# Kernel optimization log

Hardware: AMD Instinct MI355X
Metric: run time of the kernel (lower is better)

Reference implementation:

```python
import jax, jax.numpy as jnp
import numpy as np

EMB = 512
HEADS = 8
HD = EMB // HEADS
DEPTH = 6
CONT = 100
CAT_DIMS = [100] * 28
CAT = len(CAT_DIMS)
HID = int(EMB * (4.0 / 3.0))  # 682, FT-Transformer ReGLU hidden
B = 128
OFFSETS = jnp.asarray(np.concatenate([[0], np.cumsum(CAT_DIMS[:-1])]).astype(np.int32))
SQRT_EMB = float(np.sqrt(EMB))  # scores are DIVIDED by emb**-0.5 in the source


def setup_inputs() -> dict:
    key = jax.random.key(0)
    ks = jax.random.split(key, 16)
    s = 0.02
    x_cat = jax.random.randint(ks[0], (B, CAT), 0, CAT_DIMS[0]).astype(jnp.float32)
    x_cont = jax.random.normal(ks[1], (B, CONT), dtype=jnp.float32)
    x = jnp.concatenate([x_cat, x_cont], axis=1)  # [B, CAT+CONT]
    return {
        "x": x,
        "tok_w": jax.random.normal(ks[2], (CONT + 1, EMB)) * s,
        "tok_b": jax.random.normal(ks[3], (CONT + CAT, EMB)) * s,
        "cat_emb": jax.random.normal(ks[4], (sum(CAT_DIMS), EMB)) * s,
        "Wqkv": jax.random.normal(ks[5], (DEPTH, EMB, 3 * EMB)) * s,
        "bqkv": jnp.zeros((DEPTH, 3 * EMB)),
        "Wout": jax.random.normal(ks[6], (DEPTH, EMB, EMB)) * s,
        "bout": jnp.zeros((DEPTH, EMB)),
        "W0": jax.random.normal(ks[7], (DEPTH, EMB, 2 * HID)) * s,
        "b0": jnp.zeros((DEPTH, 2 * HID)),
        "W1": jax.random.normal(ks[8], (DEPTH, HID, EMB)) * s,
        "b1": jnp.zeros((DEPTH, EMB)),
        "ln0_g": jnp.ones((DEPTH, EMB)),
        "ln0_b": jnp.zeros((DEPTH, EMB)),
        "ln1_g": jnp.ones((DEPTH, EMB)),
        "ln1_b": jnp.zeros((DEPTH, EMB)),
    }


def _ln(x, g, b):
    m = x.mean(-1, keepdims=True)
    v = x.var(-1, keepdims=True)
    return (x - m) / jnp.sqrt(v + 1e-5) * g + b


def _attn(x, Wqkv, bqkv, Wout, bout):
    Bn, S, _ = x.shape
    # faithful layout: reshape to (B,S,H,3*hd), move heads, chunk last dim
    qkv = (x @ Wqkv + bqkv).reshape(Bn, S, HEADS, 3 * HD).transpose(0, 2, 1, 3)
    q, k, v = jnp.split(qkv, 3, axis=-1)  # each [B,H,S,hd]
    scores = jnp.einsum("bhqd,bhkd->bhqk", q, k) * SQRT_EMB  # / (emb**-0.5)
    attn = jax.nn.softmax(jax.nn.softmax(scores, axis=-1), axis=-1)  # double softmax, as in source
    o = jnp.einsum("bhqk,bhkd->bhqd", attn, v)
    o = o.transpose(0, 2, 1, 3).reshape(Bn, S, EMB)
    return o @ Wout + bout


def _reglu(x):
    a, b = jnp.split(x, 2, axis=-1)
    return a * jax.nn.relu(b)


def _forward(x, tok_w, tok_b, cat_emb, Wqkv, bqkv, Wout, bout, W0, b0, W1, b1,
             ln0_g, ln0_b, ln1_g, ln1_b):
    # --- feature tokenizer ---
    x_cats = x[:, :CAT].astype(jnp.int32)
    x_conts = jnp.concatenate([jnp.ones((x.shape[0], 1), x.dtype), x[:, CAT:]], axis=1)  # [B, CONT+1]
    h = tok_w[None] * x_conts[:, :, None]  # [B, CONT+1, EMB]
    h = jnp.concatenate([h, cat_emb[x_cats + OFFSETS[None]]], axis=1)  # [B, S=129, EMB]
    bias = jnp.concatenate([jnp.zeros((1, EMB), h.dtype), tok_b], axis=0)
    h = h + bias[None]
    # --- transformer stack ---
    for i in range(DEPTH):
        xin = _ln(h, ln0_g[i], ln0_b[i]) if i else h  # layer 0 has no norm0
        h = h + _attn(xin, Wqkv[i], bqkv[i], Wout[i], bout[i])
        r = _ln(h, ln1_g[i], ln1_b[i])
        r = _reglu(r @ W0[i] + b0[i]) @ W1[i] + b1[i]
        h = h + r
    return h[:, 0]  # CLS token


def reference(x, tok_w, tok_b, cat_emb, Wqkv, bqkv, Wout, bout, W0, b0, W1, b1,
              ln0_g, ln0_b, ln1_g, ln1_b):
    return _forward(x, tok_w, tok_b, cat_emb, Wqkv, bqkv, Wout, bout, W0, b0, W1, b1,
                    ln0_g, ln0_b, ln1_g, ln1_b)
```

## Files before the change

### kernel.cpp

```cpp
#include <hip/hip_runtime.h>
#include <hip/hip_bf16.h>
#include <stdint.h>


typedef __hip_bfloat16 bf16_t;
typedef __attribute__((ext_vector_type(8))) __bf16 bf16x8;
typedef __attribute__((ext_vector_type(4))) float floatx4;

constexpr int M_ROWS = 16512;
constexpr float SQRT_EMB_F = 22.627416997969522f;

__device__ __forceinline__ floatx4 mfma16(bf16x8 a, bf16x8 b, floatx4 c) {
  return __builtin_amdgcn_mfma_f32_16x16x32_bf16(a, b, c, 0, 0, 0);
}

__device__ __forceinline__ size_t frag_chunk(int m, int k, int KT) {
  return ((size_t)(m >> 4) * KT + (k >> 5)) * 512 + (m & 15) * 8 + 128 * ((k >> 3) & 3);
}
__device__ __forceinline__ size_t frag_elem(int m, int k, int KT) {
  return frag_chunk(m, k, KT) + (k & 7);
}

template <int PERM>
__global__ __launch_bounds__(256) void transpose_cvt(const float* __restrict__ W,
    bf16_t* __restrict__ WT, int K, int N, int KP, int NP)
{
  __shared__ float tile[32][33];
  int k0 = blockIdx.x * 32, n0 = blockIdx.y * 32;
  const float* Wl = W + (size_t)blockIdx.z * K * N;
  bf16_t* WTl = WT + (size_t)blockIdx.z * NP * KP;
  const int KT = KP >> 5;
  #pragma unroll
  for (int r = 0; r < 32; r += 8) {
    int k = k0 + threadIdx.y + r, n = n0 + threadIdx.x;
    int srcn = PERM ? ((n & 1) ? 682 + (n >> 1) : (n >> 1)) : n;
    int valid = (k < K) && (PERM ? (n < 1364) : (n < N));
    tile[threadIdx.y + r][threadIdx.x] = valid ? Wl[(size_t)k * N + srcn] : 0.f;
  }
  __syncthreads();
  #pragma unroll
  for (int r = 0; r < 32; r += 8) {
    int n = n0 + threadIdx.y + r, k = k0 + threadIdx.x;
    if (n < NP && k < KP)
      WTl[frag_elem(n, k, KT)] = __float2bfloat16(tile[threadIdx.x][threadIdx.y + r]);
  }
}

__global__ __launch_bounds__(256) void tokenizer_kernel(const float* __restrict__ x,
    const float* __restrict__ tok_w, const float* __restrict__ tok_b,
    const float* __restrict__ cat_emb, float* __restrict__ h, bf16_t* __restrict__ ab)
{
  int row = blockIdx.x * 4 + (threadIdx.x >> 6);
  int lane = threadIdx.x & 63, e0 = lane * 8;
  int b = row / 129, t = row - b * 129;
  float v[8];
  if (t == 0) {
    #pragma unroll
    for (int u = 0; u < 8; u++) v[u] = tok_w[e0 + u];
  } else if (t <= 100) {
    float xv = x[(size_t)b * 128 + 28 + (t - 1)];
    const float* wp = tok_w + (size_t)t * 512 + e0;
    const float* bp = tok_b + (size_t)(t - 1) * 512 + e0;
    #pragma unroll
    for (int u = 0; u < 8; u++) v[u] = wp[u] * xv + bp[u];
  } else {
    int j = t - 101;
    int idx = (int)x[(size_t)b * 128 + j] + 100 * j;
    const float* cp = cat_emb + (size_t)idx * 512 + e0;
    const float* bp = tok_b + (size_t)(t - 1) * 512 + e0;
    #pragma unroll
    for (int u = 0; u < 8; u++) v[u] = cp[u] + bp[u];
  }
  float* hr = h + (size_t)row * 512 + e0;
  #pragma unroll
  for (int u = 0; u < 8; u++) hr[u] = v[u];
  bf16x8 o8;
  #pragma unroll
  for (int u = 0; u < 8; u++) o8[u] = (__bf16)__float2bfloat16(v[u]);
  *(bf16x8*)(ab + ((size_t)(row >> 4) * 16 + (lane >> 2)) * 512 + (row & 15) * 8 + 128 * (lane & 3)) = o8;
}

__global__ __launch_bounds__(256) void ln_kernel(const float* __restrict__ hin,
    bf16_t* __restrict__ out, const float* __restrict__ g, const float* __restrict__ bta)
{
  int row = blockIdx.x * 4 + (threadIdx.x >> 6);
  int lane = threadIdx.x & 63;
  const float* hr = hin + (size_t)row * 512 + lane * 8;
  float4 v0 = *(const float4*)hr;
  float4 v1 = *(const float4*)(hr + 4);
  float s = v0.x + v0.y + v0.z + v0.w + v1.x + v1.y + v1.z + v1.w;
  float q = v0.x * v0.x + v0.y * v0.y + v0.z * v0.z + v0.w * v0.w
          + v1.x * v1.x + v1.y * v1.y + v1.z * v1.z + v1.w * v1.w;
  #pragma unroll
  for (int o = 1; o < 64; o <<= 1) { s += __shfl_xor(s, o); q += __shfl_xor(q, o); }
  float mean = s * (1.f / 512.f);
  float var = q * (1.f / 512.f) - mean * mean;
  float rstd = rsqrtf(var + 1e-5f);
  float4 g0 = *(const float4*)(g + lane * 8);
  float4 g1 = *(const float4*)(g + lane * 8 + 4);
  float4 b0v = *(const float4*)(bta + lane * 8);
  float4 b1v = *(const float4*)(bta + lane * 8 + 4);
  bf16x8 o8;
  o8[0] = (__bf16)__float2bfloat16((v0.x - mean) * rstd * g0.x + b0v.x);
  o8[1] = (__bf16)__float2bfloat16((v0.y - mean) * rstd * g0.y + b0v.y);
  o8[2] = (__bf16)__float2bfloat16((v0.z - mean) * rstd * g0.z + b0v.z);
  o8[3] = (__bf16)__float2bfloat16((v0.w - mean) * rstd * g0.w + b0v.w);
  o8[4] = (__bf16)__float2bfloat16((v1.x - mean) * rstd * g1.x + b1v.x);
  o8[5] = (__bf16)__float2bfloat16((v1.y - mean) * rstd * g1.y + b1v.y);
  o8[6] = (__bf16)__float2bfloat16((v1.z - mean) * rstd * g1.z + b1v.z);
  o8[7] = (__bf16)__float2bfloat16((v1.w - mean) * rstd * g1.w + b1v.w);
  *(bf16x8*)(out + ((size_t)(row >> 4) * 16 + (lane >> 2)) * 512 + (row & 15) * 8 + 128 * (lane & 3)) = o8;
}

template <int MODE>
__global__ __launch_bounds__(256, 3) void gemm_frag(const bf16_t* __restrict__ A,
    const bf16_t* __restrict__ BT, const float* __restrict__ bias, int biasN,
    const float* __restrict__ resid, void* __restrict__ outp, int K, int N)
{
  const int total = gridDim.x * gridDim.y;
  const int lin = blockIdx.y * gridDim.x + blockIdx.x;
  const int xcd = lin & 7, kb2 = lin >> 3;
  const int qch = total >> 3, rch = total & 7;
  const int idx = xcd * qch + (xcd < rch ? xcd : rch) + kb2;
  const int bm = idx / gridDim.x;
  const int bn = idx - bm * gridDim.x;
  const int m0 = bm * 128, n0 = bn * 128;

  const int tid = threadIdx.x;
  const int w = tid >> 6, l = tid & 63, l15 = l & 15, quad = l >> 4;
  const int wm = (w >> 1) * 64, wn = (w & 1) * 64;
  const int KT = K >> 5;

  const bf16_t* pa[4];
  const bf16_t* pb[4];
  #pragma unroll
  for (int i = 0; i < 4; i++) {
    pa[i] = A  + ((size_t)(((m0 + wm) >> 4) + i) * KT) * 512 + l * 8;
    pb[i] = BT + ((size_t)(((n0 + wn) >> 4) + i) * KT) * 512 + l * 8;
  }

  bf16x8 af[2][4], bg[2][4];
  #pragma unroll
  for (int i = 0; i < 4; i++) {
    af[0][i] = *(const bf16x8*)pa[i];
    bg[0][i] = *(const bf16x8*)pb[i];
  }

  floatx4 z4 = {0.f, 0.f, 0.f, 0.f};
  floatx4 acc[4][4];
  #pragma unroll
  for (int i = 0; i < 4; i++)
    #pragma unroll
    for (int j = 0; j < 4; j++) acc[i][j] = z4;

  const int T = KT;
  for (int t = 0; t < T; t += 2) {
    if (t + 1 < T) {
      #pragma unroll
      for (int i = 0; i < 4; i++) {
        af[1][i] = *(const bf16x8*)(pa[i] + (size_t)(t + 1) * 512);
        bg[1][i] = *(const bf16x8*)(pb[i] + (size_t)(t + 1) * 512);
      }
    }
    #pragma unroll
    for (int i = 0; i < 4; i++)
      #pragma unroll
      for (int j = 0; j < 4; j++)
        acc[i][j] = mfma16(af[0][i], bg[0][j], acc[i][j]);
    if (t + 1 < T) {
      if (t + 2 < T) {
        #pragma unroll
        for (int i = 0; i < 4; i++) {
          af[0][i] = *(const bf16x8*)(pa[i] + (size_t)(t + 2) * 512);
          bg[0][i] = *(const bf16x8*)(pb[i] + (size_t)(t + 2) * 512);
        }
      }
      #pragma unroll
      for (int i = 0; i < 4; i++)
        #pragma unroll
        for (int j = 0; j < 4; j++)
          acc[i][j] = mfma16(af[1][i], bg[1][j], acc[i][j]);
    }
  }

  #pragma unroll
  for (int j = 0; j < 4; j++) {
    int col = n0 + wn + j * 16 + l15;
    float bv = 0.f;
    if (MODE == 2) {
      if (col < biasN) bv = bias[(col & 1) ? 682 + (col >> 1) : (col >> 1)];
    } else {
      if (col < biasN) bv = bias[col];
    }
    #pragma unroll
    for (int i = 0; i < 4; i++) {
      int row_b = m0 + wm + i * 16 + quad * 4;
      #pragma unroll
      for (int r = 0; r < 4; r++) {
        float v = acc[i][j][r] + bv;
        int m = row_b + r;
        if (MODE == 2) {
          float other = __shfl_xor(v, 1);
          if (!(l15 & 1)) {
            int c2 = col >> 1;
            ((bf16_t*)outp)[frag_elem(m, c2, (N >> 1) >> 5)] =
                __float2bfloat16(v * fmaxf(other, 0.f));
          }
        } else if (MODE == 1) {
          size_t idx2 = (size_t)m * N + col;
          ((float*)outp)[idx2] = v + resid[idx2];
        } else {
          ((bf16_t*)outp)[frag_elem(m, col, N >> 5)] = __float2bfloat16(v);
        }
      }
    }
  }
}

constexpr int SPP = 168;
__global__ __launch_bounds__(320) void attn_kernel(const bf16_t* __restrict__ qkv,
                                                   bf16_t* __restrict__ attnout)
{
  __shared__ __align__(16) __bf16 vt_lds[64 * SPP];
  __shared__ __align__(16) __bf16 p_lds[5][32 * SPP];

  const int bh = blockIdx.x, b = bh >> 3, hh = bh & 7;
  const int tid = threadIdx.x;
  const int w = tid / 64, l = tid & 63, l15 = l & 15, quad = l >> 4;
  const int rbase = b * 129;

  for (int i = tid; i < 64 * SPP / 2; i += 320) ((unsigned int*)vt_lds)[i] = 0u;
  __syncthreads();
  for (int c = tid; c < 129 * 8; c += 320) {
    int s = c >> 3, ch = c & 7;
    bf16x8 tv = *(const bf16x8*)(qkv + frag_chunk(rbase + s, hh * 192 + 128 + ch * 8, 48));
    #pragma unroll
    for (int j = 0; j < 8; j++) vt_lds[(size_t)(ch * 8 + j) * SPP + s] = tv[j];
  }
  __syncthreads();

  const int qt = w;
  __bf16* pw = p_lds[w];

  bf16x8 zq = {};
  bf16x8 aq[2][2];
  #pragma unroll
  for (int mt = 0; mt < 2; mt++) {
    int m = qt * 32 + mt * 16 + l15;
    #pragma unroll
    for (int t = 0; t < 2; t++)
      aq[mt][t] = (m < 129)
          ? *(const bf16x8*)(qkv + frag_chunk(rbase + m, hh * 192 + t * 32 + quad * 8, 48)) : zq;
  }

  floatx4 z4 = {0.f, 0.f, 0.f, 0.f};
  floatx4 sc[2][9];
  #pragma unroll
  for (int mt = 0; mt < 2; mt++)
    #pragma unroll
    for (int nt = 0; nt < 9; nt++) sc[mt][nt] = z4;
  #pragma unroll
  for (int nt = 0; nt < 9; nt++) {
    int krow = nt * 16 + l15;
    #pragma unroll
    for (int t = 0; t < 2; t++) {
      bf16x8 kf = (krow < 129)
          ? *(const bf16x8*)(qkv + frag_chunk(rbase + krow, hh * 192 + 64 + t * 32 + quad * 8, 48))
          : zq;
      sc[0][nt] = mfma16(aq[0][t], kf, sc[0][nt]);
      sc[1][nt] = mfma16(aq[1][t], kf, sc[1][nt]);
    }
  }

  const bool v8 = (l15 == 0);
  #pragma unroll
  for (int mt = 0; mt < 2; mt++) {
    #pragma unroll
    for (int r = 0; r < 4; r++) {
      float v[9];
      #pragma unroll
      for (int nt = 0; nt < 9; nt++) v[nt] = sc[mt][nt][r] * SQRT_EMB_F;
      float mx = -1e30f;
      #pragma unroll
      for (int nt = 0; nt < 8; nt++) mx = fmaxf(mx, v[nt]);
      if (v8) mx = fmaxf(mx, v[8]);
      #pragma unroll
      for (int o = 1; o < 16; o <<= 1) mx = fmaxf(mx, __shfl_xor(mx, o));
      float sum = 0.f;
      #pragma unroll
      for (int nt = 0; nt < 8; nt++) { v[nt] = __expf(v[nt] - mx); sum += v[nt]; }
      v[8] = v8 ? __expf(v[8] - mx) : 0.f;
      sum += v[8];
      #pragma unroll
      for (int o = 1; o < 16; o <<= 1) sum += __shfl_xor(sum, o);
      float inv = 1.f / sum;
      float mx2 = 0.f;
      #pragma unroll
      for (int nt = 0; nt < 9; nt++) { v[nt] *= inv; mx2 = fmaxf(mx2, v[nt]); }
      #pragma unroll
      for (int o = 1; o < 16; o <<= 1) mx2 = fmaxf(mx2, __shfl_xor(mx2, o));
      float sum2 = 0.f;
      #pragma unroll
      for (int nt = 0; nt < 8; nt++) { v[nt] = __expf(v[nt] - mx2); sum2 += v[nt]; }
      v[8] = v8 ? __expf(v[8] - mx2) : 0.f;
      sum2 += v[8];
      #pragma unroll
      for (int o = 1; o < 16; o <<= 1) sum2 += __shfl_xor(sum2, o);
      float inv2 = 1.f / sum2;
      int row = mt * 16 + quad * 4 + r;
      #pragma unroll
      for (int nt = 0; nt < 9; nt++) {
        float pv = (nt < 8 || v8) ? v[nt] * inv2 : 0.f;
        pw[(size_t)row * SPP + nt * 16 + l15] = __bf16(__float2bfloat16(pv));
      }
      pw[(size_t)row * SPP + 144 + l15] = __bf16(0.0f);
    }
  }
  asm volatile("" ::: "memory");

  floatx4 oacc[2][4];
  #pragma unroll
  for (int mt = 0; mt < 2; mt++)
    #pragma unroll
    for (int dt = 0; dt < 4; dt++) oacc[mt][dt] = z4;
  #pragma unroll
  for (int kt = 0; kt < 5; kt++) {
    bf16x8 pf[2], vf[4];
    #pragma unroll
    for (int mt = 0; mt < 2; mt++)
      pf[mt] = *(const bf16x8*)&pw[(size_t)(mt * 16 + l15) * SPP + kt * 32 + quad * 8];
    #pragma unroll
    for (int dt = 0; dt < 4; dt++)
      vf[dt] = *(const bf16x8*)&vt_lds[(size_t)(dt * 16 + l15) * SPP + kt * 32 + quad * 8];
    #pragma unroll
    for (int mt = 0; mt < 2; mt++)
      #pragma unroll
      for (int dt = 0; dt < 4; dt++)
        oacc[mt][dt] = mfma16(pf[mt], vf[dt], oacc[mt][dt]);
  }
  #pragma unroll
  for (int mt = 0; mt < 2; mt++)
    #pragma unroll
    for (int dt = 0; dt < 4; dt++)
      #pragma unroll
      for (int r = 0; r < 4; r++) {
        int sq = qt * 32 + mt * 16 + quad * 4 + r;
        if (sq < 129) {
          int cc = hh * 64 + dt * 16 + l15;
          attnout[frag_elem(rbase + sq, cc, 16)] = __float2bfloat16(oacc[mt][dt][r]);
        }
      }
}

__global__ __launch_bounds__(256) void out_copy(const float* __restrict__ h,
                                                float* __restrict__ out)
{
  int b = blockIdx.x, e = threadIdx.x;
  out[(size_t)b * 512 + e]       = h[(size_t)b * 129 * 512 + e];
  out[(size_t)b * 512 + e + 256] = h[(size_t)b * 129 * 512 + e + 256];
}

extern "C" void kernel_launch(void* const* d_in, const int* in_sizes, int n_in,
                              void* d_out, int out_size, void* d_ws, size_t ws_size,
                              hipStream_t stream)
{
  const float* x       = (const float*)d_in[0];
  const float* tok_w   = (const float*)d_in[1];
  const float* tok_b   = (const float*)d_in[2];
  const float* cat_emb = (const float*)d_in[3];
  const float* Wqkv    = (const float*)d_in[4];
  const float* bqkv    = (const float*)d_in[5];
  const float* Wout    = (const float*)d_in[6];
  const float* bout    = (const float*)d_in[7];
  const float* W0      = (const float*)d_in[8];
  const float* b0      = (const float*)d_in[9];
  const float* W1      = (const float*)d_in[10];
  const float* b1      = (const float*)d_in[11];
  const float* ln0_g   = (const float*)d_in[12];
  const float* ln0_b   = (const float*)d_in[13];
  const float* ln1_g   = (const float*)d_in[14];
  const float* ln1_b   = (const float*)d_in[15];

  size_t off = 0;
  char* base = (char*)d_ws;
  auto alloc = [&](size_t n) { char* p = base + off; off += (n + 255) & ~(size_t)255; return p; };
  float*  h     = (float*) alloc((size_t)M_ROWS * 512 * 4);
  bf16_t* ab    = (bf16_t*)alloc((size_t)M_ROWS * 512 * 2);
  bf16_t* qkv   = (bf16_t*)alloc((size_t)M_ROWS * 1536 * 2);
  bf16_t* attno = (bf16_t*)alloc((size_t)M_ROWS * 512 * 2);
  bf16_t* regl  = (bf16_t*)alloc((size_t)M_ROWS * 704 * 2);
  bf16_t* WqkvT = (bf16_t*)alloc((size_t)6 * 1536 * 512 * 2);
  bf16_t* WoutT = (bf16_t*)alloc((size_t)6 * 512 * 512 * 2);
  bf16_t* W0T   = (bf16_t*)alloc((size_t)6 * 1408 * 512 * 2);
  bf16_t* W1T   = (bf16_t*)alloc((size_t)6 * 512 * 704 * 2);
  (void)ws_size; (void)in_sizes; (void)n_in; (void)out_size;

  dim3 tb(32, 8, 1);
  transpose_cvt<0><<<dim3(16, 48, 6), tb, 0, stream>>>(Wqkv, WqkvT, 512, 1536, 512, 1536);
  transpose_cvt<0><<<dim3(16, 16, 6), tb, 0, stream>>>(Wout, WoutT, 512, 512, 512, 512);
  transpose_cvt<1><<<dim3(16, 44, 6), tb, 0, stream>>>(W0, W0T, 512, 1364, 512, 1408);
  transpose_cvt<0><<<dim3(22, 16, 6), tb, 0, stream>>>(W1, W1T, 682, 512, 704, 512);

  tokenizer_kernel<<<M_ROWS / 4, 256, 0, stream>>>(x, tok_w, tok_b, cat_emb, h, ab);

  for (int i = 0; i < 6; i++) {
    if (i)
      ln_kernel<<<M_ROWS / 4, 256, 0, stream>>>(h, ab, ln0_g + (size_t)i * 512,
                                                ln0_b + (size_t)i * 512);
    gemm_frag<0><<<dim3(12, 129), 256, 0, stream>>>(
        ab, WqkvT + (size_t)i * 1536 * 512, bqkv + (size_t)i * 1536, 1536, nullptr, qkv, 512, 1536);
    attn_kernel<<<1024, 320, 0, stream>>>(qkv, attno);
    gemm_frag<1><<<dim3(4, 129), 256, 0, stream>>>(
        attno, WoutT + (size_t)i * 512 * 512, bout + (size_t)i * 512, 512, h, h, 512, 512);
    ln_kernel<<<M_ROWS / 4, 256, 0, stream>>>(h, ab, ln1_g + (size_t)i * 512,
                                              ln1_b + (size_t)i * 512);
    gemm_frag<2><<<dim3(11, 129), 256, 0, stream>>>(
        ab, W0T + (size_t)i * 1408 * 512, b0 + (size_t)i * 1364, 1364, nullptr, regl, 512, 1408);
    gemm_frag<1><<<dim3(4, 129), 256, 0, stream>>>(
        regl, W1T + (size_t)i * 512 * 704, b1 + (size_t)i * 512, 512, h, h, 704, 512);
  }

  out_copy<<<128, 256, 0, stream>>>(h, (float*)d_out);
}
```

Measured before the change: 1.358 ms.

## Widen GEMM tiles to 128x256 and transpose attention MFMA layout

The GEMM kernel now computes 128x256 output tiles, with each wave holding 4x8 accumulators. This doubles B-fragment reuse per A load and halves the grid, with padded W0/W1 widths of 1536 and 768 so the tile divides N. The attention kernel computes S^T so softmax reductions span only two cross-quad shuffles. P and V^T are stored in LDS in MFMA fragment layout, so PV uses contiguous 16-byte loads and outputs are written as bf16x4 vectors. The risks are much higher register pressure (launch bounds 1), wasted work on padded columns, and fewer blocks for the small-N GEMMs.

```diff
diff --git a/kernel.cpp b/kernel.cpp
--- a/kernel.cpp
+++ b/kernel.cpp
@@ -5,6 +5,7 @@
 
 typedef __hip_bfloat16 bf16_t;
 typedef __attribute__((ext_vector_type(8))) __bf16 bf16x8;
+typedef __attribute__((ext_vector_type(4))) __bf16 bf16x4;
 typedef __attribute__((ext_vector_type(4))) float floatx4;
 
 constexpr int M_ROWS = 16512;
@@ -113,7 +114,7 @@
 }
 
 template <int MODE>
-__global__ __launch_bounds__(256, 3) void gemm_frag(const bf16_t* __restrict__ A,
+__global__ __launch_bounds__(256, 1) void gemm_big(const bf16_t* __restrict__ A,
     const bf16_t* __restrict__ BT, const float* __restrict__ bias, int biasN,
     const float* __restrict__ resid, void* __restrict__ outp, int K, int N)
 {
@@ -124,67 +125,65 @@
   const int idx = xcd * qch + (xcd < rch ? xcd : rch) + kb2;
   const int bm = idx / gridDim.x;
   const int bn = idx - bm * gridDim.x;
-  const int m0 = bm * 128, n0 = bn * 128;
+  const int m0 = bm * 128, n0 = bn * 256;
 
   const int tid = threadIdx.x;
   const int w = tid >> 6, l = tid & 63, l15 = l & 15, quad = l >> 4;
-  const int wm = (w >> 1) * 64, wn = (w & 1) * 64;
+  const int wm = (w >> 1) * 64, wn = (w & 1) * 128;
   const int KT = K >> 5;
 
   const bf16_t* pa[4];
-  const bf16_t* pb[4];
-  #pragma unroll
-  for (int i = 0; i < 4; i++) {
-    pa[i] = A  + ((size_t)(((m0 + wm) >> 4) + i) * KT) * 512 + l * 8;
-    pb[i] = BT + ((size_t)(((n0 + wn) >> 4) + i) * KT) * 512 + l * 8;
-  }
-
-  bf16x8 af[2][4], bg[2][4];
-  #pragma unroll
-  for (int i = 0; i < 4; i++) {
-    af[0][i] = *(const bf16x8*)pa[i];
-    bg[0][i] = *(const bf16x8*)pb[i];
-  }
+  const bf16_t* pb[8];
+  #pragma unroll
+  for (int i = 0; i < 4; i++)
+    pa[i] = A + ((size_t)(((m0 + wm) >> 4) + i) * KT) * 512 + l * 8;
+  #pragma unroll
+  for (int j = 0; j < 8; j++)
+    pb[j] = BT + ((size_t)(((n0 + wn) >> 4) + j) * KT) * 512 + l * 8;
+
+  bf16x8 af[2][4], bg[2][8];
+  #pragma unroll
+  for (int i = 0; i < 4; i++) af[0][i] = *(const bf16x8*)pa[i];
+  #pragma unroll
+  for (int j = 0; j < 8; j++) bg[0][j] = *(const bf16x8*)pb[j];
 
   floatx4 z4 = {0.f, 0.f, 0.f, 0.f};
-  floatx4 acc[4][4];
+  floatx4 acc[4][8];
   #pragma unroll
   for (int i = 0; i < 4; i++)
     #pragma unroll
-    for (int j = 0; j < 4; j++) acc[i][j] = z4;
+    for (int j = 0; j < 8; j++) acc[i][j] = z4;
 
   const int T = KT;
   for (int t = 0; t < T; t += 2) {
     if (t + 1 < T) {
       #pragma unroll
-      for (int i = 0; i < 4; i++) {
-        af[1][i] = *(const bf16x8*)(pa[i] + (size_t)(t + 1) * 512);
-        bg[1][i] = *(const bf16x8*)(pb[i] + (size_t)(t + 1) * 512);
-      }
+      for (int i = 0; i < 4; i++) af[1][i] = *(const bf16x8*)(pa[i] + (size_t)(t + 1) * 512);
+      #pragma unroll
+      for (int j = 0; j < 8; j++) bg[1][j] = *(const bf16x8*)(pb[j] + (size_t)(t + 1) * 512);
     }
     #pragma unroll
     for (int i = 0; i < 4; i++)
       #pragma unroll
-      for (int j = 0; j < 4; j++)
+      for (int j = 0; j < 8; j++)
         acc[i][j] = mfma16(af[0][i], bg[0][j], acc[i][j]);
     if (t + 1 < T) {
       if (t + 2 < T) {
         #pragma unroll
-        for (int i = 0; i < 4; i++) {
-          af[0][i] = *(const bf16x8*)(pa[i] + (size_t)(t + 2) * 512);
-          bg[0][i] = *(const bf16x8*)(pb[i] + (size_t)(t + 2) * 512);
-        }
+        for (int i = 0; i < 4; i++) af[0][i] = *(const bf16x8*)(pa[i] + (size_t)(t + 2) * 512);
+        #pragma unroll
+        for (int j = 0; j < 8; j++) bg[0][j] = *(const bf16x8*)(pb[j] + (size_t)(t + 2) * 512);
       }
       #pragma unroll
       for (int i = 0; i < 4; i++)
         #pragma unroll
-        for (int j = 0; j < 4; j++)
+        for (int j = 0; j < 8; j++)
           acc[i][j] = mfma16(af[1][i], bg[1][j], acc[i][j]);
     }
   }
 
   #pragma unroll
-  for (int j = 0; j < 4; j++) {
+  for (int j = 0; j < 8; j++) {
     int col = n0 + wn + j * 16 + l15;
     float bv = 0.f;
     if (MODE == 2) {
@@ -217,30 +216,30 @@
   }
 }
 
-constexpr int SPP = 168;
-__global__ __launch_bounds__(320) void attn_kernel(const bf16_t* __restrict__ qkv,
-                                                   bf16_t* __restrict__ attnout)
-{
-  __shared__ __align__(16) __bf16 vt_lds[64 * SPP];
-  __shared__ __align__(16) __bf16 p_lds[5][32 * SPP];
+__global__ __launch_bounds__(320, 3) void attn_kernel(const bf16_t* __restrict__ qkv,
+                                                      bf16_t* __restrict__ attnout)
+{
+  __shared__ __align__(16) __bf16 vt[4 * 5 * 512];
+  __shared__ __align__(16) __bf16 pbuf[5][5 * 512];
 
   const int bh = blockIdx.x, b = bh >> 3, hh = bh & 7;
   const int tid = threadIdx.x;
-  const int w = tid / 64, l = tid & 63, l15 = l & 15, quad = l >> 4;
+  const int w = tid >> 6, l = tid & 63, l15 = l & 15, quad = l >> 4;
   const int rbase = b * 129;
-
-  for (int i = tid; i < 64 * SPP / 2; i += 320) ((unsigned int*)vt_lds)[i] = 0u;
+  const int qt = w;
+  __bf16* pw = pbuf[w];
+
+  for (int i = tid; i < 4 * 5 * 512 / 2; i += 320) ((unsigned int*)vt)[i] = 0u;
   __syncthreads();
   for (int c = tid; c < 129 * 8; c += 320) {
     int s = c >> 3, ch = c & 7;
     bf16x8 tv = *(const bf16x8*)(qkv + frag_chunk(rbase + s, hh * 192 + 128 + ch * 8, 48));
-    #pragma unroll
-    for (int j = 0; j < 8; j++) vt_lds[(size_t)(ch * 8 + j) * SPP + s] = tv[j];
+    int kc = s >> 5, s31 = s & 31;
+    int base = ((ch >> 1) * 5 + kc) * 512 + 128 * (s31 >> 3) + (s31 & 7) + (ch & 1) * 64;
+    #pragma unroll
+    for (int j = 0; j < 8; j++) vt[base + j * 8] = tv[j];
   }
   __syncthreads();
-
-  const int qt = w;
-  __bf16* pw = p_lds[w];
 
   bf16x8 zq = {};
   bf16x8 aq[2][2];
@@ -254,102 +253,113 @@
   }
 
   floatx4 z4 = {0.f, 0.f, 0.f, 0.f};
-  floatx4 sc[2][9];
+  floatx4 sT[2][9];
   #pragma unroll
   for (int mt = 0; mt < 2; mt++)
     #pragma unroll
-    for (int nt = 0; nt < 9; nt++) sc[mt][nt] = z4;
-  #pragma unroll
-  for (int nt = 0; nt < 9; nt++) {
-    int krow = nt * 16 + l15;
+    for (int st = 0; st < 9; st++) sT[mt][st] = z4;
+  #pragma unroll
+  for (int st = 0; st < 9; st++) {
+    int srow = st * 16 + l15;
     #pragma unroll
     for (int t = 0; t < 2; t++) {
-      bf16x8 kf = (krow < 129)
-          ? *(const bf16x8*)(qkv + frag_chunk(rbase + krow, hh * 192 + 64 + t * 32 + quad * 8, 48))
+      bf16x8 kf = (srow < 129)
+          ? *(const bf16x8*)(qkv + frag_chunk(rbase + srow, hh * 192 + 64 + t * 32 + quad * 8, 48))
           : zq;
-      sc[0][nt] = mfma16(aq[0][t], kf, sc[0][nt]);
-      sc[1][nt] = mfma16(aq[1][t], kf, sc[1][nt]);
-    }
-  }
-
-  const bool v8 = (l15 == 0);
+      sT[0][st] = mfma16(kf, aq[0][t], sT[0][st]);
+      sT[1][st] = mfma16(kf, aq[1][t], sT[1][st]);
+    }
+  }
+
+  const bool val8 = (quad == 0);
   #pragma unroll
   for (int mt = 0; mt < 2; mt++) {
-    #pragma unroll
-    for (int r = 0; r < 4; r++) {
-      float v[9];
-      #pragma unroll
-      for (int nt = 0; nt < 9; nt++) v[nt] = sc[mt][nt][r] * SQRT_EMB_F;
-      float mx = -1e30f;
-      #pragma unroll
-      for (int nt = 0; nt < 8; nt++) mx = fmaxf(mx, v[nt]);
-      if (v8) mx = fmaxf(mx, v[8]);
-      #pragma unroll
-      for (int o = 1; o < 16; o <<= 1) mx = fmaxf(mx, __shfl_xor(mx, o));
-      float sum = 0.f;
-      #pragma unroll
-      for (int nt = 0; nt < 8; nt++) { v[nt] = __expf(v[nt] - mx); sum += v[nt]; }
-      v[8] = v8 ? __expf(v[8] - mx) : 0.f;
-      sum += v[8];
-      #pragma unroll
-      for (int o = 1; o < 16; o <<= 1) sum += __shfl_xor(sum, o);
-      float inv = 1.f / sum;
-      float mx2 = 0.f;
-      #pragma unroll
-      for (int nt = 0; nt < 9; nt++) { v[nt] *= inv; mx2 = fmaxf(mx2, v[nt]); }
-      #pragma unroll
-      for (int o = 1; o < 16; o <<= 1) mx2 = fmaxf(mx2, __shfl_xor(mx2, o));
-      float sum2 = 0.f;
-      #pragma unroll
-      for (int nt = 0; nt < 8; nt++) { v[nt] = __expf(v[nt] - mx2); sum2 += v[nt]; }
-      v[8] = v8 ? __expf(v[8] - mx2) : 0.f;
-      sum2 += v[8];
-      #pragma unroll
-      for (int o = 1; o < 16; o <<= 1) sum2 += __shfl_xor(sum2, o);
-      float inv2 = 1.f / sum2;
-      int row = mt * 16 + quad * 4 + r;
-      #pragma unroll
-      for (int nt = 0; nt < 9; nt++) {
-        float pv = (nt < 8 || v8) ? v[nt] * inv2 : 0.f;
-        pw[(size_t)row * SPP + nt * 16 + l15] = __bf16(__float2bfloat16(pv));
+    float v[9][4];
+    #pragma unroll
+    for (int st = 0; st < 9; st++)
+      #pragma unroll
+      for (int r = 0; r < 4; r++) v[st][r] = sT[mt][st][r] * SQRT_EMB_F;
+    float mx = -3e38f;
+    #pragma unroll
+    for (int st = 0; st < 8; st++)
+      #pragma unroll
+      for (int r = 0; r < 4; r++) mx = fmaxf(mx, v[st][r]);
+    if (val8) mx = fmaxf(mx, v[8][0]);
+    mx = fmaxf(mx, __shfl_xor(mx, 16));
+    mx = fmaxf(mx, __shfl_xor(mx, 32));
+    float sum = 0.f;
+    #pragma unroll
+    for (int st = 0; st < 8; st++)
+      #pragma unroll
+      for (int r = 0; r < 4; r++) { v[st][r] = __expf(v[st][r] - mx); sum += v[st][r]; }
+    v[8][0] = val8 ? __expf(v[8][0] - mx) : 0.f;
+    v[8][1] = v[8][2] = v[8][3] = 0.f;
+    sum += v[8][0];
+    sum += __shfl_xor(sum, 16);
+    sum += __shfl_xor(sum, 32);
+    float inv = 1.f / sum;
+    float mx2 = 0.f;
+    #pragma unroll
+    for (int st = 0; st < 8; st++)
+      #pragma unroll
+      for (int r = 0; r < 4; r++) { v[st][r] *= inv; mx2 = fmaxf(mx2, v[st][r]); }
+    v[8][0] *= inv; mx2 = fmaxf(mx2, v[8][0]);
+    mx2 = fmaxf(mx2, __shfl_xor(mx2, 16));
+    mx2 = fmaxf(mx2, __shfl_xor(mx2, 32));
+    float sum2 = 0.f;
+    #pragma unroll
+    for (int st = 0; st < 8; st++)
+      #pragma unroll
+      for (int r = 0; r < 4; r++) { v[st][r] = __expf(v[st][r] - mx2); sum2 += v[st][r]; }
+    v[8][0] = val8 ? __expf(v[8][0] - mx2) : 0.f;
+    sum2 += v[8][0];
+    sum2 += __shfl_xor(sum2, 16);
+    sum2 += __shfl_xor(sum2, 32);
+    float inv2 = 1.f / sum2;
+
+    #pragma unroll
+    for (int st = 0; st < 9; st++) {
+      bf16x4 t4;
+      #pragma unroll
+      for (int r = 0; r < 4; r++) t4[r] = (__bf16)__float2bfloat16(v[st][r] * inv2);
+      int off = (st >> 1) * 512 + l15 * 8 + 128 * ((st & 1) * 2 + (quad >> 1)) + (quad & 1) * 4;
+      *(bf16x4*)&pw[off] = t4;
+    }
+    {
+      bf16x4 t4;
+      #pragma unroll
+      for (int r = 0; r < 4; r++) t4[r] = (__bf16)__float2bfloat16(0.f);
+      int off = 4 * 512 + l15 * 8 + 128 * (2 + (quad >> 1)) + (quad & 1) * 4;
+      *(bf16x4*)&pw[off] = t4;
+    }
+    __builtin_amdgcn_s_waitcnt(0xC07F);
+    asm volatile("" ::: "memory");
+
+    floatx4 oacc[4];
+    #pragma unroll
+    for (int dt = 0; dt < 4; dt++) oacc[dt] = z4;
+    #pragma unroll
+    for (int kc = 0; kc < 5; kc++) {
+      bf16x8 pf = *(const bf16x8*)&pw[kc * 512 + l * 8];
+      #pragma unroll
+      for (int dt = 0; dt < 4; dt++) {
+        bf16x8 vf = *(const bf16x8*)&vt[(dt * 5 + kc) * 512 + l * 8];
+        oacc[dt] = mfma16(vf, pf, oacc[dt]);
       }
-      pw[(size_t)row * SPP + 144 + l15] = __bf16(0.0f);
-    }
-  }
-  asm volatile("" ::: "memory");
-
-  floatx4 oacc[2][4];
-  #pragma unroll
-  for (int mt = 0; mt < 2; mt++)
-    #pragma unroll
-    for (int dt = 0; dt < 4; dt++) oacc[mt][dt] = z4;
-  #pragma unroll
-  for (int kt = 0; kt < 5; kt++) {
-    bf16x8 pf[2], vf[4];
-    #pragma unroll
-    for (int mt = 0; mt < 2; mt++)
-      pf[mt] = *(const bf16x8*)&pw[(size_t)(mt * 16 + l15) * SPP + kt * 32 + quad * 8];
-    #pragma unroll
-    for (int dt = 0; dt < 4; dt++)
-      vf[dt] = *(const bf16x8*)&vt_lds[(size_t)(dt * 16 + l15) * SPP + kt * 32 + quad * 8];
-    #pragma unroll
-    for (int mt = 0; mt < 2; mt++)
-      #pragma unroll
-      for (int dt = 0; dt < 4; dt++)
-        oacc[mt][dt] = mfma16(pf[mt], vf[dt], oacc[mt][dt]);
-  }
-  #pragma unroll
-  for (int mt = 0; mt < 2; mt++)
-    #pragma unroll
-    for (int dt = 0; dt < 4; dt++)
-      #pragma unroll
-      for (int r = 0; r < 4; r++) {
-        int sq = qt * 32 + mt * 16 + quad * 4 + r;
-        if (sq < 129) {
-          int cc = hh * 64 + dt * 16 + l15;
-          attnout[frag_elem(rbase + sq, cc, 16)] = __float2bfloat16(oacc[mt][dt][r]);
-        }
+    }
+    int m = qt * 32 + mt * 16 + l15;
+    if (m < 129) {
+      #pragma unroll
+      for (int dt = 0; dt < 4; dt++) {
+        int c0 = hh * 64 + dt * 16 + quad * 4;
+        bf16x4 t4;
+        #pragma unroll
+        for (int r = 0; r < 4; r++) t4[r] = (__bf16)__float2bfloat16(oacc[dt][r]);
+        *(bf16x4*)(attnout + frag_elem(rbase + m, c0, 16)) = t4;
       }
+    }
+    asm volatile("" ::: "memory");
+  }
 }
 
 __global__ __launch_bounds__(256) void out_copy(const float* __restrict__ h,
@@ -388,18 +398,18 @@
   bf16_t* ab    = (bf16_t*)alloc((size_t)M_ROWS * 512 * 2);
   bf16_t* qkv   = (bf16_t*)alloc((size_t)M_ROWS * 1536 * 2);
   bf16_t* attno = (bf16_t*)alloc((size_t)M_ROWS * 512 * 2);
-  bf16_t* regl  = (bf16_t*)alloc((size_t)M_ROWS * 704 * 2);
+  bf16_t* regl  = (bf16_t*)alloc((size_t)M_ROWS * 768 * 2);
   bf16_t* WqkvT = (bf16_t*)alloc((size_t)6 * 1536 * 512 * 2);
   bf16_t* WoutT = (bf16_t*)alloc((size_t)6 * 512 * 512 * 2);
-  bf16_t* W0T   = (bf16_t*)alloc((size_t)6 * 1408 * 512 * 2);
-  bf16_t* W1T   = (bf16_t*)alloc((size_t)6 * 512 * 704 * 2);
+  bf16_t* W0T   = (bf16_t*)alloc((size_t)6 * 1536 * 512 * 2);
+  bf16_t* W1T   = (bf16_t*)alloc((size_t)6 * 512 * 768 * 2);
   (void)ws_size; (void)in_sizes; (void)n_in; (void)out_size;
 
   dim3 tb(32, 8, 1);
   transpose_cvt<0><<<dim3(16, 48, 6), tb, 0, stream>>>(Wqkv, WqkvT, 512, 1536, 512, 1536);
   transpose_cvt<0><<<dim3(16, 16, 6), tb, 0, stream>>>(Wout, WoutT, 512, 512, 512, 512);
-  transpose_cvt<1><<<dim3(16, 44, 6), tb, 0, stream>>>(W0, W0T, 512, 1364, 512, 1408);
-  transpose_cvt<0><<<dim3(22, 16, 6), tb, 0, stream>>>(W1, W1T, 682, 512, 704, 512);
+  transpose_cvt<1><<<dim3(16, 48, 6), tb, 0, stream>>>(W0, W0T, 512, 1364, 512, 1536);
+  transpose_cvt<0><<<dim3(24, 16, 6), tb, 0, stream>>>(W1, W1T, 682, 512, 768, 512);
 
   tokenizer_kernel<<<M_ROWS / 4, 256, 0, stream>>>(x, tok_w, tok_b, cat_emb, h, ab);
 
@@ -407,17 +417,17 @@
     if (i)
       ln_kernel<<<M_ROWS / 4, 256, 0, stream>>>(h, ab, ln0_g + (size_t)i * 512,
                                                 ln0_b + (size_t)i * 512);
-    gemm_frag<0><<<dim3(12, 129), 256, 0, stream>>>(
+    gemm_big<0><<<dim3(6, 129), 256, 0, stream>>>(
         ab, WqkvT + (size_t)i * 1536 * 512, bqkv + (size_t)i * 1536, 1536, nullptr, qkv, 512, 1536);
     attn_kernel<<<1024, 320, 0, stream>>>(qkv, attno);
-    gemm_frag<1><<<dim3(4, 129), 256, 0, stream>>>(
+    gemm_big<1><<<dim3(2, 129), 256, 0, stream>>>(
         attno, WoutT + (size_t)i * 512 * 512, bout + (size_t)i * 512, 512, h, h, 512, 512);
     ln_kernel<<<M_ROWS / 4, 256, 0, stream>>>(h, ab, ln1_g + (size_t)i * 512,
                                               ln1_b + (size_t)i * 512);
-    gemm_frag<2><<<dim3(11, 129), 256, 0, stream>>>(
-        ab, W0T + (size_t)i * 1408 * 512, b0 + (size_t)i * 1364, 1364, nullptr, regl, 512, 1408);
-    gemm_frag<1><<<dim3(4, 129), 256, 0, stream>>>(
-        regl, W1T + (size_t)i * 512 * 704, b1 + (size_t)i * 512, 512, h, h, 704, 512);
+    gemm_big<2><<<dim3(6, 129), 256, 0, stream>>>(
+        ab, W0T + (size_t)i * 1536 * 512, b0 + (size_t)i * 1364, 1364, nullptr, regl, 512, 1536);
+    gemm_big<1><<<dim3(2, 129), 256, 0, stream>>>(
+        regl, W1T + (size_t)i * 512 * 768, b1 + (size_t)i * 512, 512, h, h, 768, 512);
   }
 
   out_copy<<<128, 256, 0, stream>>>(h, (float*)d_out);
```

Result: slower. 1.761 ms (+29.7%).
